# Kernel optimization log

Measured on AMD Instinct MI355X. Metric: run time of the kernel, lower is better.

The kernel has to match this reference:

```python
import jax, jax.numpy as jnp
import numpy as np

GROUP = 64  # group_size for precision='int4'


def setup_inputs() -> dict:
    key = jax.random.key(0)
    ks = jax.random.split(key, 7)
    B, S, C, O, R = 64, 4, 8192, 8192, 32
    x = jax.random.normal(ks[0], (B, S, C), dtype=jnp.float32)
    # unpacked int4 weight values stored as int32 codes in [0,16) -> value = code - 8
    qweight = jax.random.randint(ks[1], (O, C), 0, 16, dtype=jnp.int32)
    wscales = jax.random.uniform(ks[2], (C // GROUP, O), dtype=jnp.float32,
                                 minval=0.005, maxval=0.02)
    # smoothing factors kept strictly positive and away from zero
    smooth_factor = jax.random.uniform(ks[3], (C,), dtype=jnp.float32,
                                       minval=0.5, maxval=1.5)
    proj_down = jax.random.normal(ks[4], (C, R), dtype=jnp.float32) * 0.02
    proj_up = jax.random.normal(ks[5], (O, R), dtype=jnp.float32) * 0.02
    bias = jax.random.normal(ks[6], (O,), dtype=jnp.float32) * 0.01
    return {"x": x, "qweight": qweight, "wscales": wscales,
            "smooth_factor": smooth_factor, "proj_down": proj_down,
            "proj_up": proj_up, "bias": bias}


def reference(x, qweight, wscales, smooth_factor, proj_down, proj_up, bias):
    B, S, C = x.shape
    O = qweight.shape[0]
    ng = C // GROUP
    xr = x.reshape(B * S, C)

    # SVD low-rank correction: lora_act = x @ proj_down ; out += lora_act @ proj_up^T
    lora = (xr @ proj_down) @ proj_up.T  # (M, O)

    # activation smoothing + per-group symmetric int4 quantization
    xs = xr / smooth_factor                                   # (M, C)
    xg = xs.reshape(-1, ng, GROUP)                            # (M, ng, 64)
    ascales = jnp.max(jnp.abs(xg), axis=-1, keepdims=True) / 7.0
    ascales = jnp.maximum(ascales, 1e-8)
    q_act = jnp.clip(jnp.round(xg / ascales), -8.0, 7.0)
    x_deq = (q_act * ascales).reshape(-1, C)                  # dequantized act

    # per-group weight dequant: wscales is (ng, O)
    w = (qweight.astype(jnp.float32) - 8.0).reshape(O, ng, GROUP)
    w_deq = (w * wscales.T[:, :, None]).reshape(O, C)         # (O, C)

    out = x_deq @ w_deq.T + lora + bias                       # (M, O)
    return out.reshape(B, S, O)
```

## Files before the change

kernel.cpp:

```cpp
#include <hip/hip_runtime.h>
#include <stdint.h>

#define C_DIM 8192
#define O_DIM 8192
#define M_DIM 256
#define NG    128
#define NGH   64
#define SUPS  8
#define RK    32

typedef float f32x4 __attribute__((ext_vector_type(4)));
typedef int   i32x4 __attribute__((ext_vector_type(4)));
typedef unsigned int u32;

__device__ __forceinline__ void gll16(const void* g, void* l) {
  __builtin_amdgcn_global_load_lds(
      (const __attribute__((address_space(1))) void*)g,
      (__attribute__((address_space(3))) void*)l, 16, 0, 0);
}
__device__ __forceinline__ int pack4(int a, int b, int c, int d) {
  return (a & 0xff) | ((b & 0xff) << 8) | ((c & 0xff) << 16) | (d << 24);
}

__global__ __launch_bounds__(256) void k_lora(const float* __restrict__ x,
                                              const float* __restrict__ pd,
                                              float* __restrict__ lact) {
  const int t  = threadIdx.x;
  const int rq = t & 7;
  const int kc = (t >> 3) & 15;
  const int ml = t >> 7;
  const int m  = blockIdx.x * 2 + ml;
  const float* xrow = x + (size_t)m * C_DIM + kc * 512;
  const float* pdp  = pd + (size_t)(kc * 512) * RK + rq * 4;
  float a0 = 0.f, a1 = 0.f, a2 = 0.f, a3 = 0.f;
  for (int k = 0; k < 512; k += 4) {
    float4 xv = *(const float4*)(xrow + k);
    float4 p0 = *(const float4*)(pdp + (size_t)(k + 0) * RK);
    float4 p1 = *(const float4*)(pdp + (size_t)(k + 1) * RK);
    float4 p2 = *(const float4*)(pdp + (size_t)(k + 2) * RK);
    float4 p3 = *(const float4*)(pdp + (size_t)(k + 3) * RK);
    a0 += xv.x * p0.x + xv.y * p1.x + xv.z * p2.x + xv.w * p3.x;
    a1 += xv.x * p0.y + xv.y * p1.y + xv.z * p2.y + xv.w * p3.y;
    a2 += xv.x * p0.z + xv.y * p1.z + xv.z * p2.z + xv.w * p3.z;
    a3 += xv.x * p0.w + xv.y * p1.w + xv.z * p2.w + xv.w * p3.w;
  }
  __shared__ float red[2][8][16][4];
  red[ml][rq][kc][0] = a0;
  red[ml][rq][kc][1] = a1;
  red[ml][rq][kc][2] = a2;
  red[ml][rq][kc][3] = a3;
  __syncthreads();
  if (t < 64) {
    const int ml2 = t >> 5, r = t & 31, rq2 = r >> 2, j = r & 3;
    float s = 0.f;
#pragma unroll
    for (int c = 0; c < 16; ++c) s += red[ml2][rq2][c][j];
    lact[(size_t)(blockIdx.x * 2 + ml2) * RK + r] = s;
  }
}

__global__ __launch_bounds__(256) void k_prep(const float* __restrict__ x,
                                              const float* __restrict__ smooth,
                                              float* __restrict__ scp,
                                              i32x4* __restrict__ wsA8) {
  const int t    = threadIdx.x;
  const int ml   = t & 15;
  const int gl   = t >> 4;
  const int MT   = blockIdx.x >> 3;
  const int gblk = blockIdx.x & 7;
  const int m = MT * 16 + ml;
  const int g = gblk * 16 + gl;
  const float* xp = x + (size_t)m * C_DIM + g * 64;
  const float* sp = smooth + g * 64;
  float xs[64];
  float amax = 0.0f;
#pragma unroll
  for (int i = 0; i < 64; i += 4) {
    float4 xv = *(const float4*)(xp + i);
    float4 sv = *(const float4*)(sp + i);
    xs[i + 0] = xv.x / sv.x;
    xs[i + 1] = xv.y / sv.y;
    xs[i + 2] = xv.z / sv.z;
    xs[i + 3] = xv.w / sv.w;
    amax = fmaxf(amax, fabsf(xs[i + 0]));
    amax = fmaxf(amax, fabsf(xs[i + 1]));
    amax = fmaxf(amax, fabsf(xs[i + 2]));
    amax = fmaxf(amax, fabsf(xs[i + 3]));
  }
  const float ascale = fmaxf(amax / 7.0f, 1e-8f);
  int qi[64];
  int rs = 0;
#pragma unroll
  for (int i = 0; i < 64; ++i) {
    float qv = fminf(fmaxf(rintf(xs[i] / ascale), -8.0f), 7.0f);
    qi[i] = (int)qv;
    rs += qi[i];
  }
  scp[(size_t)g * 512 + m]       = ascale;
  scp[(size_t)g * 512 + 256 + m] = 8.0f * (float)rs * ascale;
  const size_t base = ((size_t)(MT * NG + g)) * 64;
#pragma unroll
  for (int lg = 0; lg < 4; ++lg) {
    const int* q = qi + lg * 16;
    i32x4 c;
#pragma unroll
    for (int dw = 0; dw < 4; ++dw)
      c[dw] = pack4(q[dw * 4 + 0], q[dw * 4 + 1], q[dw * 4 + 2], q[dw * 4 + 3]);
    wsA8[base + lg * 16 + ml] = c;
  }
}

__global__ __launch_bounds__(512, 2) void k_main(
    const int* __restrict__ qw, const float* __restrict__ wsc,
    const float* __restrict__ scp, const i32x4* __restrict__ wsA8,
    float* __restrict__ P) {
  const int t    = threadIdx.x;
  const int bid  = blockIdx.x;
  const int kh   = bid & 1;
  const int n0   = (bid >> 1) * 32;
  const int g0   = kh * NGH;
  const int w    = t >> 6;
  const int l    = t & 63;
  const int lrow = l >> 4;
  const int lcol = l & 15;

  __shared__ char  ldsB[2][32 * 528];
  __shared__ float ldsSC[2][4096];
  __shared__ float ldsW[NGH * 32];

  for (int i = t; i < NGH * 32; i += 512)
    ldsW[i] = wsc[(size_t)(g0 + (i >> 5)) * O_DIM + n0 + (i & 31)];

  const int sr = t >> 4, sc = t & 15;
  const int* gB = qw + (size_t)(n0 + sr) * C_DIM + kh * 4096 + sc * 32;
  const float* gSC = scp + (size_t)g0 * 512 + t * 4;
  const int wOff = sr * 528 + sc * 32;
  const i32x4* gA0 = wsA8 + ((size_t)(w * 2 + 0) * NG + g0) * 64 + l;
  const i32x4* gA1 = wsA8 + ((size_t)(w * 2 + 1) * NG + g0) * 64 + l;

  __syncthreads();

  i32x4 br0, br1, br2, br3, br4, br5, br6, br7;
  i32x4 R0_0, R0_1, R1_0, R1_1, R2_0, R2_1, R3_0, R3_1;

#define LOADB(S)                                                               \
  br0 = *(const i32x4*)(gB + (S) * 512 + 0);                                   \
  br1 = *(const i32x4*)(gB + (S) * 512 + 4);                                   \
  br2 = *(const i32x4*)(gB + (S) * 512 + 8);                                   \
  br3 = *(const i32x4*)(gB + (S) * 512 + 12);                                  \
  br4 = *(const i32x4*)(gB + (S) * 512 + 16);                                  \
  br5 = *(const i32x4*)(gB + (S) * 512 + 20);                                  \
  br6 = *(const i32x4*)(gB + (S) * 512 + 24);                                  \
  br7 = *(const i32x4*)(gB + (S) * 512 + 28);
#define LOADSC(S, BUF)                                                         \
  gll16(gSC + (size_t)(S) * 4096, &ldsSC[BUF][t * 4]);                         \
  gll16(gSC + (size_t)(S) * 4096 + 2048, &ldsSC[BUF][2048 + t * 4]);
#define PACKW(BUF)                                                             \
  {                                                                            \
    i32x4 pk0, pk1;                                                            \
    pk0[0] = pack4(br0[0], br0[1], br0[2], br0[3]);                            \
    pk0[1] = pack4(br1[0], br1[1], br1[2], br1[3]);                            \
    pk0[2] = pack4(br2[0], br2[1], br2[2], br2[3]);                            \
    pk0[3] = pack4(br3[0], br3[1], br3[2], br3[3]);                            \
    pk1[0] = pack4(br4[0], br4[1], br4[2], br4[3]);                            \
    pk1[1] = pack4(br5[0], br5[1], br5[2], br5[3]);                            \
    pk1[2] = pack4(br6[0], br6[1], br6[2], br6[3]);                            \
    pk1[3] = pack4(br7[0], br7[1], br7[2], br7[3]);                            \
    *(i32x4*)&ldsB[BUF][wOff] = pk0;                                           \
    *(i32x4*)&ldsB[BUF][wOff + 16] = pk1;                                      \
  }

  LOADB(0)
  LOADSC(0, 0)
  R0_0 = gA0[0 * 64];  R0_1 = gA1[0 * 64];
  R1_0 = gA0[1 * 64];  R1_1 = gA1[1 * 64];
  R2_0 = gA0[2 * 64];  R2_1 = gA1[2 * 64];
  R3_0 = gA0[3 * 64];  R3_1 = gA1[3 * 64];
  asm volatile("s_waitcnt vmcnt(8)" ::: "memory");
  PACKW(0)
  asm volatile("s_waitcnt lgkmcnt(0)" ::: "memory");
  __builtin_amdgcn_s_barrier();

  f32x4 acc00 = (f32x4){0.f, 0.f, 0.f, 0.f};
  f32x4 acc01 = (f32x4){0.f, 0.f, 0.f, 0.f};
  f32x4 acc10 = (f32x4){0.f, 0.f, 0.f, 0.f};
  f32x4 acc11 = (f32x4){0.f, 0.f, 0.f, 0.f};
  const i32x4 z = (i32x4){0, 0, 0, 0};

#define SUBJ(J, RA0, RA1, VMC)                                                 \
  {                                                                            \
    asm volatile("s_waitcnt vmcnt(" #VMC ")" ::: "memory");                    \
    const char* bb = &ldsB[s & 1][0];                                          \
    i32x4 bf0 = *(const i32x4*)(bb + lcol * 528 + (J) * 64 + lrow * 16);       \
    i32x4 bf1 = *(const i32x4*)(bb + (16 + lcol) * 528 + (J) * 64 + lrow * 16);\
    const float* scb = &ldsSC[s & 1][(J) * 512];                               \
    f32x4 as0 = *(const f32x4*)(scb + (w * 2 + 0) * 16 + lrow * 4);            \
    f32x4 rs0 = *(const f32x4*)(scb + 256 + (w * 2 + 0) * 16 + lrow * 4);      \
    f32x4 as1 = *(const f32x4*)(scb + (w * 2 + 1) * 16 + lrow * 4);            \
    f32x4 rs1 = *(const f32x4*)(scb + 256 + (w * 2 + 1) * 16 + lrow * 4);      \
    const float wsv0 = ldsW[(s * 8 + (J)) * 32 + lcol];                        \
    const float wsv1 = ldsW[(s * 8 + (J)) * 32 + 16 + lcol];                   \
    i32x4 d00 = __builtin_amdgcn_mfma_i32_16x16x64_i8(RA0, bf0, z, 0, 0, 0);   \
    i32x4 d01 = __builtin_amdgcn_mfma_i32_16x16x64_i8(RA0, bf1, z, 0, 0, 0);   \
    i32x4 d10 = __builtin_amdgcn_mfma_i32_16x16x64_i8(RA1, bf0, z, 0, 0, 0);   \
    i32x4 d11 = __builtin_amdgcn_mfma_i32_16x16x64_i8(RA1, bf1, z, 0, 0, 0);   \
    {                                                                          \
      int lgn = s * 8 + (J) + 4;                                               \
      if (lgn > NGH - 1) lgn = NGH - 1;                                        \
      RA0 = gA0[(size_t)lgn * 64];                                             \
      RA1 = gA1[(size_t)lgn * 64];                                             \
    }                                                                          \
    f32x4 df;                                                                  \
    df[0] = (float)d00[0]; df[1] = (float)d00[1];                              \
    df[2] = (float)d00[2]; df[3] = (float)d00[3];                              \
    acc00 += wsv0 * (as0 * df - rs0);                                          \
    df[0] = (float)d01[0]; df[1] = (float)d01[1];                              \
    df[2] = (float)d01[2]; df[3] = (float)d01[3];                              \
    acc01 += wsv1 * (as0 * df - rs0);                                          \
    df[0] = (float)d10[0]; df[1] = (float)d10[1];                              \
    df[2] = (float)d10[2]; df[3] = (float)d10[3];                              \
    acc10 += wsv0 * (as1 * df - rs1);                                          \
    df[0] = (float)d11[0]; df[1] = (float)d11[1];                              \
    df[2] = (float)d11[2]; df[3] = (float)d11[3];                              \
    acc11 += wsv1 * (as1 * df - rs1);                                          \
  }

  for (int s = 0; s < SUPS; ++s) {
    const int sn = (s < SUPS - 1) ? s + 1 : SUPS - 1;
    const int nb = (s + 1) & 1;
    LOADB(sn)
    LOADSC(sn, nb)
    SUBJ(0, R0_0, R0_1, 16)
    SUBJ(1, R1_0, R1_1, 16)
    SUBJ(2, R2_0, R2_1, 16)
    SUBJ(3, R3_0, R3_1, 16)
    SUBJ(4, R0_0, R0_1, 6)
    SUBJ(5, R1_0, R1_1, 6)
    SUBJ(6, R2_0, R2_1, 6)
    SUBJ(7, R3_0, R3_1, 6)
    asm volatile("s_waitcnt vmcnt(8)" ::: "memory");
    PACKW(nb)
    asm volatile("s_waitcnt lgkmcnt(0)" ::: "memory");
    __builtin_amdgcn_s_barrier();
  }
#undef SUBJ
#undef LOADB
#undef LOADSC
#undef PACKW

  float* Pk = P + (size_t)kh * (M_DIM * O_DIM);
#pragma unroll
  for (int mi = 0; mi < 2; ++mi) {
#pragma unroll
    for (int ni = 0; ni < 2; ++ni) {
      const f32x4 av = (mi == 0) ? (ni == 0 ? acc00 : acc01)
                                 : (ni == 0 ? acc10 : acc11);
      const int n = n0 + ni * 16 + lcol;
#pragma unroll
      for (int j = 0; j < 4; ++j) {
        const int m = (w * 2 + mi) * 16 + lrow * 4 + j;
        Pk[(size_t)m * O_DIM + n] = av[j];
      }
    }
  }
}

__global__ __launch_bounds__(256) void k_red(const float* __restrict__ P,
                                             const float* __restrict__ lact,
                                             const float* __restrict__ pu,
                                             const float* __restrict__ bias,
                                             float* __restrict__ out) {
  const int t  = threadIdx.x;
  const int tn = t & 31;
  const int tm = t >> 5;
  const int n0 = blockIdx.x * 32;
  __shared__ float puL[32][33];
  for (int i = t; i < 1024; i += 256)
    puL[i >> 5][i & 31] = pu[(size_t)(n0 + (i >> 5)) * RK + (i & 31)];
  __syncthreads();
  const int n = n0 + tn;
  const float bv = bias[n];
  for (int m = tm; m < M_DIM; m += 8) {
    const float* lp = lact + (size_t)m * RK;
    float s = bv;
#pragma unroll
    for (int r = 0; r < 32; r += 4) {
      float4 lv = *(const float4*)(lp + r);
      s += lv.x * puL[tn][r] + lv.y * puL[tn][r + 1] + lv.z * puL[tn][r + 2] +
           lv.w * puL[tn][r + 3];
    }
    const size_t o = (size_t)m * O_DIM + n;
    out[o] = P[o] + P[(size_t)M_DIM * O_DIM + o] + s;
  }
}

extern "C" void kernel_launch(void* const* d_in, const int* in_sizes, int n_in,
                              void* d_out, int out_size, void* d_ws,
                              size_t ws_size, hipStream_t stream) {
  const float* x      = (const float*)d_in[0];
  const int*   qw     = (const int*)d_in[1];
  const float* wsc    = (const float*)d_in[2];
  const float* smooth = (const float*)d_in[3];
  const float* pd     = (const float*)d_in[4];
  const float* pu     = (const float*)d_in[5];
  const float* bias   = (const float*)d_in[6];
  float* out = (float*)d_out;

  char* ws = (char*)d_ws;
  float* lact = (float*)ws;
  float* scp  = (float*)(ws + 32 * 1024);
  i32x4* wsA8 = (i32x4*)(ws + 288 * 1024);
  float* P    = (float*)(ws + 2336 * 1024);

  hipLaunchKernelGGL(k_prep, dim3(128), dim3(256), 0, stream, x, smooth, scp,
                     wsA8);
  hipLaunchKernelGGL(k_lora, dim3(128), dim3(256), 0, stream, x, pd, lact);
  hipLaunchKernelGGL(k_main, dim3(512), dim3(512), 0, stream, qw, wsc, scp,
                     wsA8, P);
  hipLaunchKernelGGL(k_red, dim3(256), dim3(256), 0, stream, P, lact, pu, bias,
                     out);
}
```

Before: 192.7 us.

## Prepack int4 weights to MFMA-tiled int8 layout and fuse reduction epilogue

Adds a separate k_pack kernel that converts the int32 weight codes into a tiled int8 layout matching the MFMA B-fragment order. The new main kernel streams that layout straight into LDS with global_load_lds, so the in-loop pack step and the padded LDS writes go away. Each block now covers all 128 groups instead of a K-half, which drops the partial-sum buffer and the separate reduction kernel. Bias and the LoRA up-projection are applied in the main kernel's epilogue. The cost is an extra full pass over the 256MB weight tensor every call, a larger workspace requirement, and half as many blocks in the main kernel.

```diff
diff --git a/kernel.cpp b/kernel.cpp
--- a/kernel.cpp
+++ b/kernel.cpp
@@ -6,7 +6,6 @@
 #define M_DIM 256
 #define NG    128
 #define NGH   64
-#define SUPS  8
 #define RK    32
 
 typedef float f32x4 __attribute__((ext_vector_type(4)));
@@ -20,6 +19,33 @@
 }
 __device__ __forceinline__ int pack4(int a, int b, int c, int d) {
   return (a & 0xff) | ((b & 0xff) << 8) | ((c & 0xff) << 16) | (d << 24);
+}
+
+__global__ __launch_bounds__(256) void k_pack(const int* __restrict__ qw,
+                                              char* __restrict__ qp) {
+  const int t    = threadIdx.x;
+  const int row  = blockIdx.x * 4 + (t >> 6);
+  const int c0   = t & 63;
+  const int nslab = row >> 5, nloc = row & 31;
+  const int nt = nloc >> 4, lcol = nloc & 15;
+  const size_t rbase = (size_t)row * C_DIM;
+  const size_t wbase = ((size_t)nslab * NG) * 2048 + nt * 1024 + lcol * 16;
+#pragma unroll
+  for (int i = 0; i < 8; ++i) {
+    const int c = c0 + i * 64;
+    const int* src = qw + rbase + (size_t)c * 16;
+    i32x4 r0 = __builtin_nontemporal_load((const i32x4*)(src));
+    i32x4 r1 = __builtin_nontemporal_load((const i32x4*)(src + 4));
+    i32x4 r2 = __builtin_nontemporal_load((const i32x4*)(src + 8));
+    i32x4 r3 = __builtin_nontemporal_load((const i32x4*)(src + 12));
+    i32x4 pk;
+    pk[0] = pack4(r0[0], r0[1], r0[2], r0[3]);
+    pk[1] = pack4(r1[0], r1[1], r1[2], r1[3]);
+    pk[2] = pack4(r2[0], r2[1], r2[2], r2[3]);
+    pk[3] = pack4(r3[0], r3[1], r3[2], r3[3]);
+    const int g = c >> 2, lr = c & 3;
+    *(i32x4*)(qp + wbase + (size_t)g * 2048 + lr * 256) = pk;
+  }
 }
 
 __global__ __launch_bounds__(256) void k_lora(const float* __restrict__ x,
@@ -110,39 +136,170 @@
   }
 }
 
-__global__ __launch_bounds__(512, 2) void k_main(
-    const int* __restrict__ qw, const float* __restrict__ wsc,
+__global__ __launch_bounds__(512, 2) void k_mainQ(
+    const char* __restrict__ qp, const float* __restrict__ wsc,
+    const float* __restrict__ pu, const float* __restrict__ bias,
     const float* __restrict__ scp, const i32x4* __restrict__ wsA8,
-    float* __restrict__ P) {
+    const float* __restrict__ lact, float* __restrict__ out) {
   const int t    = threadIdx.x;
-  const int bid  = blockIdx.x;
-  const int kh   = bid & 1;
-  const int n0   = (bid >> 1) * 32;
-  const int g0   = kh * NGH;
+  const int n0   = blockIdx.x * 32;
   const int w    = t >> 6;
   const int l    = t & 63;
   const int lrow = l >> 4;
   const int lcol = l & 15;
 
-  __shared__ char  ldsB[2][32 * 528];
+  __shared__ char  ldsB[2][16384];
+  __shared__ float ldsSC[2][4096];
+  __shared__ float ldsW[NG * 32];
+
+  for (int i = t; i < NG * 32; i += 512)
+    ldsW[i] = wsc[(size_t)(i >> 5) * O_DIM + n0 + (i & 31)];
+
+  const char*  qpB = qp + (size_t)blockIdx.x * (NG * 2048);
+  const float* gSC = scp + t * 4;
+  const i32x4* gA0 = wsA8 + ((size_t)(w * 2 + 0) * NG) * 64 + l;
+  const i32x4* gA1 = wsA8 + ((size_t)(w * 2 + 1) * NG) * 64 + l;
+
+  __syncthreads();
+
+  i32x4 R0a, R0b, R1a, R1b, R2a, R2b, R3a, R3b;
+  i32x4 R4a, R4b, R5a, R5b, R6a, R6b, R7a, R7b;
+
+  gll16(qpB + t * 16, &ldsB[0][t * 16]);
+  gll16(qpB + 8192 + t * 16, &ldsB[0][8192 + t * 16]);
+  gll16(gSC, &ldsSC[0][t * 4]);
+  gll16(gSC + 2048, &ldsSC[0][2048 + t * 4]);
+  R0a = gA0[0 * 64];  R0b = gA1[0 * 64];
+  R1a = gA0[1 * 64];  R1b = gA1[1 * 64];
+  R2a = gA0[2 * 64];  R2b = gA1[2 * 64];
+  R3a = gA0[3 * 64];  R3b = gA1[3 * 64];
+  R4a = gA0[4 * 64];  R4b = gA1[4 * 64];
+  R5a = gA0[5 * 64];  R5b = gA1[5 * 64];
+  R6a = gA0[6 * 64];  R6b = gA1[6 * 64];
+  R7a = gA0[7 * 64];  R7b = gA1[7 * 64];
+  asm volatile("s_waitcnt vmcnt(16)" ::: "memory");
+  __builtin_amdgcn_s_barrier();
+
+  f32x4 acc00 = (f32x4){0.f, 0.f, 0.f, 0.f};
+  f32x4 acc01 = (f32x4){0.f, 0.f, 0.f, 0.f};
+  f32x4 acc10 = (f32x4){0.f, 0.f, 0.f, 0.f};
+  f32x4 acc11 = (f32x4){0.f, 0.f, 0.f, 0.f};
+  const i32x4 z = (i32x4){0, 0, 0, 0};
+
+#define SUBJ(J, RA, RB)                                                        \
+  {                                                                            \
+    asm volatile("s_waitcnt vmcnt(18)" ::: "memory");                          \
+    const char* bb = &ldsB[s & 1][(J) * 2048];                                 \
+    i32x4 bf0 = *(const i32x4*)(bb + l * 16);                                  \
+    i32x4 bf1 = *(const i32x4*)(bb + 1024 + l * 16);                           \
+    const float* scb = &ldsSC[s & 1][(J) * 512];                               \
+    f32x4 as0 = *(const f32x4*)(scb + (w * 2 + 0) * 16 + lrow * 4);            \
+    f32x4 rs0 = *(const f32x4*)(scb + 256 + (w * 2 + 0) * 16 + lrow * 4);      \
+    f32x4 as1 = *(const f32x4*)(scb + (w * 2 + 1) * 16 + lrow * 4);            \
+    f32x4 rs1 = *(const f32x4*)(scb + 256 + (w * 2 + 1) * 16 + lrow * 4);      \
+    const float wsv0 = ldsW[(s * 8 + (J)) * 32 + lcol];                        \
+    const float wsv1 = ldsW[(s * 8 + (J)) * 32 + 16 + lcol];                   \
+    i32x4 d00 = __builtin_amdgcn_mfma_i32_16x16x64_i8(RA, bf0, z, 0, 0, 0);    \
+    i32x4 d01 = __builtin_amdgcn_mfma_i32_16x16x64_i8(RA, bf1, z, 0, 0, 0);    \
+    i32x4 d10 = __builtin_amdgcn_mfma_i32_16x16x64_i8(RB, bf0, z, 0, 0, 0);    \
+    i32x4 d11 = __builtin_amdgcn_mfma_i32_16x16x64_i8(RB, bf1, z, 0, 0, 0);    \
+    {                                                                          \
+      int lgn = s * 8 + (J) + 8;                                               \
+      if (lgn > NG - 1) lgn = NG - 1;                                          \
+      RA = gA0[(size_t)lgn * 64];                                              \
+      RB = gA1[(size_t)lgn * 64];                                              \
+    }                                                                          \
+    f32x4 df;                                                                  \
+    df[0] = (float)d00[0]; df[1] = (float)d00[1];                              \
+    df[2] = (float)d00[2]; df[3] = (float)d00[3];                              \
+    acc00 += wsv0 * (as0 * df - rs0);                                          \
+    df[0] = (float)d01[0]; df[1] = (float)d01[1];                              \
+    df[2] = (float)d01[2]; df[3] = (float)d01[3];                              \
+    acc01 += wsv1 * (as0 * df - rs0);                                          \
+    df[0] = (float)d10[0]; df[1] = (float)d10[1];                              \
+    df[2] = (float)d10[2]; df[3] = (float)d10[3];                              \
+    acc10 += wsv0 * (as1 * df - rs1);                                          \
+    df[0] = (float)d11[0]; df[1] = (float)d11[1];                              \
+    df[2] = (float)d11[2]; df[3] = (float)d11[3];                              \
+    acc11 += wsv1 * (as1 * df - rs1);                                          \
+  }
+
+  for (int s = 0; s < 16; ++s) {
+    const int sn = (s < 15) ? s + 1 : 15;
+    const int nb = (s + 1) & 1;
+    gll16(qpB + (size_t)sn * 16384 + t * 16, &ldsB[nb][t * 16]);
+    gll16(qpB + (size_t)sn * 16384 + 8192 + t * 16, &ldsB[nb][8192 + t * 16]);
+    gll16(gSC + (size_t)sn * 4096, &ldsSC[nb][t * 4]);
+    gll16(gSC + (size_t)sn * 4096 + 2048, &ldsSC[nb][2048 + t * 4]);
+    SUBJ(0, R0a, R0b)
+    SUBJ(1, R1a, R1b)
+    SUBJ(2, R2a, R2b)
+    SUBJ(3, R3a, R3b)
+    SUBJ(4, R4a, R4b)
+    SUBJ(5, R5a, R5b)
+    SUBJ(6, R6a, R6b)
+    SUBJ(7, R7a, R7b)
+    asm volatile("s_waitcnt vmcnt(16)" ::: "memory");
+    __builtin_amdgcn_s_barrier();
+  }
+#undef SUBJ
+
+#pragma unroll
+  for (int ni = 0; ni < 2; ++ni) {
+    const int n = n0 + ni * 16 + lcol;
+    const float bv = bias[n];
+    float4 puq[8];
+#pragma unroll
+    for (int rq = 0; rq < 8; ++rq)
+      puq[rq] = *(const float4*)(pu + (size_t)n * RK + rq * 4);
+#pragma unroll
+    for (int mi = 0; mi < 2; ++mi) {
+      const f32x4 av = (mi == 0) ? (ni == 0 ? acc00 : acc01)
+                                 : (ni == 0 ? acc10 : acc11);
+#pragma unroll
+      for (int j = 0; j < 4; ++j) {
+        const int m = (w * 2 + mi) * 16 + lrow * 4 + j;
+        const float* lp = lact + (size_t)m * RK;
+        float lo = 0.f;
+#pragma unroll
+        for (int rq = 0; rq < 8; ++rq) {
+          float4 lv = *(const float4*)(lp + rq * 4);
+          lo += lv.x * puq[rq].x + lv.y * puq[rq].y + lv.z * puq[rq].z +
+                lv.w * puq[rq].w;
+        }
+        out[(size_t)m * O_DIM + n] = av[j] + bv + lo;
+      }
+    }
+  }
+}
+
+__global__ __launch_bounds__(512, 2) void k_mainF(
+    const int* __restrict__ qw, const float* __restrict__ wsc,
+    const float* __restrict__ scp, const i32x4* __restrict__ wsA8,
+    float* __restrict__ P) {
+  const int t = threadIdx.x;
+  const int bid = blockIdx.x;
+  const int kh = bid & 1;
+  const int n0 = (bid >> 1) * 32;
+  const int g0 = kh * NGH;
+  const int w = t >> 6;
+  const int l = t & 63;
+  const int lrow = l >> 4;
+  const int lcol = l & 15;
+  __shared__ char ldsB[2][32 * 528];
   __shared__ float ldsSC[2][4096];
   __shared__ float ldsW[NGH * 32];
-
   for (int i = t; i < NGH * 32; i += 512)
     ldsW[i] = wsc[(size_t)(g0 + (i >> 5)) * O_DIM + n0 + (i & 31)];
-
   const int sr = t >> 4, sc = t & 15;
   const int* gB = qw + (size_t)(n0 + sr) * C_DIM + kh * 4096 + sc * 32;
   const float* gSC = scp + (size_t)g0 * 512 + t * 4;
   const int wOff = sr * 528 + sc * 32;
   const i32x4* gA0 = wsA8 + ((size_t)(w * 2 + 0) * NG + g0) * 64 + l;
   const i32x4* gA1 = wsA8 + ((size_t)(w * 2 + 1) * NG + g0) * 64 + l;
-
   __syncthreads();
-
   i32x4 br0, br1, br2, br3, br4, br5, br6, br7;
   i32x4 R0_0, R0_1, R1_0, R1_1, R2_0, R2_1, R3_0, R3_1;
-
 #define LOADB(S)                                                               \
   br0 = *(const i32x4*)(gB + (S) * 512 + 0);                                   \
   br1 = *(const i32x4*)(gB + (S) * 512 + 4);                                   \
@@ -169,7 +326,6 @@
     *(i32x4*)&ldsB[BUF][wOff] = pk0;                                           \
     *(i32x4*)&ldsB[BUF][wOff + 16] = pk1;                                      \
   }
-
   LOADB(0)
   LOADSC(0, 0)
   R0_0 = gA0[0 * 64];  R0_1 = gA1[0 * 64];
@@ -180,13 +336,11 @@
   PACKW(0)
   asm volatile("s_waitcnt lgkmcnt(0)" ::: "memory");
   __builtin_amdgcn_s_barrier();
-
   f32x4 acc00 = (f32x4){0.f, 0.f, 0.f, 0.f};
   f32x4 acc01 = (f32x4){0.f, 0.f, 0.f, 0.f};
   f32x4 acc10 = (f32x4){0.f, 0.f, 0.f, 0.f};
   f32x4 acc11 = (f32x4){0.f, 0.f, 0.f, 0.f};
   const i32x4 z = (i32x4){0, 0, 0, 0};
-
 #define SUBJ(J, RA0, RA1, VMC)                                                 \
   {                                                                            \
     asm volatile("s_waitcnt vmcnt(" #VMC ")" ::: "memory");                    \
@@ -224,9 +378,8 @@
     df[2] = (float)d11[2]; df[3] = (float)d11[3];                              \
     acc11 += wsv1 * (as1 * df - rs1);                                          \
   }
-
-  for (int s = 0; s < SUPS; ++s) {
-    const int sn = (s < SUPS - 1) ? s + 1 : SUPS - 1;
+  for (int s = 0; s < 8; ++s) {
+    const int sn = (s < 7) ? s + 1 : 7;
     const int nb = (s + 1) & 1;
     LOADB(sn)
     LOADSC(sn, nb)
@@ -247,7 +400,6 @@
 #undef LOADB
 #undef LOADSC
 #undef PACKW
-
   float* Pk = P + (size_t)kh * (M_DIM * O_DIM);
 #pragma unroll
   for (int mi = 0; mi < 2; ++mi) {
@@ -310,13 +462,26 @@
   float* lact = (float*)ws;
   float* scp  = (float*)(ws + 32 * 1024);
   i32x4* wsA8 = (i32x4*)(ws + 288 * 1024);
-  float* P    = (float*)(ws + 2336 * 1024);
-
-  hipLaunchKernelGGL(k_prep, dim3(128), dim3(256), 0, stream, x, smooth, scp,
-                     wsA8);
-  hipLaunchKernelGGL(k_lora, dim3(128), dim3(256), 0, stream, x, pd, lact);
-  hipLaunchKernelGGL(k_main, dim3(512), dim3(512), 0, stream, qw, wsc, scp,
-                     wsA8, P);
-  hipLaunchKernelGGL(k_red, dim3(256), dim3(256), 0, stream, P, lact, pu, bias,
-                     out);
-}
+  char*  big  = ws + 2336 * 1024;
+
+  const bool bigok = ws_size >= (size_t)(2336 * 1024) + (size_t)64 * 1024 * 1024;
+
+  if (bigok) {
+    char* qp = big;
+    hipLaunchKernelGGL(k_pack, dim3(2048), dim3(256), 0, stream, qw, qp);
+    hipLaunchKernelGGL(k_prep, dim3(128), dim3(256), 0, stream, x, smooth, scp,
+                       wsA8);
+    hipLaunchKernelGGL(k_lora, dim3(128), dim3(256), 0, stream, x, pd, lact);
+    hipLaunchKernelGGL(k_mainQ, dim3(256), dim3(512), 0, stream, qp, wsc, pu,
+                       bias, scp, wsA8, lact, out);
+  } else {
+    float* P = (float*)big;
+    hipLaunchKernelGGL(k_prep, dim3(128), dim3(256), 0, stream, x, smooth, scp,
+                       wsA8);
+    hipLaunchKernelGGL(k_lora, dim3(128), dim3(256), 0, stream, x, pd, lact);
+    hipLaunchKernelGGL(k_mainF, dim3(512), dim3(512), 0, stream, qw, wsc, scp,
+                       wsA8, P);
+    hipLaunchKernelGGL(k_red, dim3(256), dim3(256), 0, stream, P, lact, pu,
+                       bias, out);
+  }
+}
```

Measured after the change: 319.0 us. 1.66x slower.
